# Optimization experiments

Measured on AMD Instinct MI355X. Metric: run time of the kernel, lower is better.

Reference implementation:

```python
import jax, jax.numpy as jnp
import numpy as np

SQRT_2_OVER_PI = 0.7978845608028654

def gelu_tanh(x):
    return 0.5 * x * (1.0 + jnp.tanh(SQRT_2_OVER_PI * (x + 0.044715 * x ** 3)))

def setup_inputs() -> dict:
    key = jax.random.key(0)
    ks = jax.random.split(key, 16)
    B, L, H, Dk, Dv = 4, 512, 8, 64, 64
    dm = H * Dk
    inp = {
        'q': jax.random.normal(ks[0], (B, L, dm), jnp.float32),
        'k': jax.random.normal(ks[1], (B, L, dm), jnp.float32),
        'v': jax.random.normal(ks[2], (B, L, dm), jnp.float32),
        'vec_adj_k': jax.random.normal(ks[3], (B, L, L, Dk), jnp.float32),
        'vec_adj_v': jax.random.normal(ks[4], (B, L, L, Dv), jnp.float32),
        'adj_k': jax.random.randint(ks[5], (B, L, L), 0, 2, jnp.int32),
        'adj_v': jax.random.randint(ks[6], (B, L, L), 0, 2, jnp.int32),
        # learned params (Linear weights stored as [in, out]; y = x @ W)
        'w_qs': jax.random.normal(ks[7], (dm, H * Dk), jnp.float32) * 0.02,
        'w_ks': jax.random.normal(ks[8], (dm, H * Dk), jnp.float32) * 0.02,
        'w_vs': jax.random.normal(ks[9], (dm, H * Dv), jnp.float32) * 0.02,
        'w_fc': jax.random.normal(ks[10], (H * Dk, H * Dk), jnp.float32) * 0.02,
        'w_nw': jax.random.normal(ks[11], (H * Dk, 1), jnp.float32) * 0.02,
        'w_self': jax.random.normal(ks[12], (H * Dk, H * Dk), jnp.float32) * 0.02,
        'w_dd': jax.random.normal(ks[13], (H * Dk, H * Dk), jnp.float32) * 0.02,
    }
    return inp

def reference(q, k, v, vec_adj_k, vec_adj_v, adj_k, adj_v,
              w_qs, w_ks, w_vs, w_fc, w_nw, w_self, w_dd):
    H, Dk, Dv = 8, 64, 64
    B, L, dm = q.shape
    temperature = Dk ** 0.5
    residual = q
    # projections -> [B, H, L, D]
    qh = (q @ w_qs).reshape(B, L, H, Dk).transpose(0, 2, 1, 3)
    kh = (k @ w_ks).reshape(B, L, H, Dk).transpose(0, 2, 1, 3)
    vh = (v @ w_vs).reshape(B, L, H, Dv).transpose(0, 2, 1, 3)
    qs = qh / temperature
    # inner_(q, k, vec_adj_k, flag=True): content + relative-position scores
    scores = jnp.einsum('bhld,bhmd->bhlm', qs, kh) \
           + jnp.einsum('bhld,blmd->bhlm', qs, vec_adj_k)  # [B,H,L,L]
    # adjacency mask (mask == 0 -> -10000)
    scores = jnp.where(adj_k[:, None, :, :] == 0, jnp.float32(-10000.0), scores)
    attn = jax.nn.softmax(scores, axis=-1)
    # inner_(attn, v, vec_adj_v, flag=False)
    out = jnp.einsum('bhlm,bhmd->bhld', attn, vh) \
        + jnp.einsum('bhlm,blmd->bhld', attn, vec_adj_v)
    qc = out.transpose(0, 2, 1, 3).reshape(B, L, H * Dv)  # [B,L,dm]
    # masked neighbor aggregation (GNN stage)
    adj_f = adj_k.astype(qc.dtype)
    nn_num = adj_f.sum(-1)                                  # [B,L]
    denom = jnp.where(nn_num >= 1.0, nn_num, 1.0)
    node_weight = jax.nn.sigmoid((qc @ w_nw)[..., 0])       # [B,L]
    self_info = qc @ w_self
    dd_info = qc @ w_dd
    dd_weight = node_weight[:, None, :] * adj_f             # [B,L,L]
    agg = jnp.matmul(dd_weight, dd_info) / denom[..., None]
    qo = gelu_tanh((self_info + agg) @ w_fc)
    qo = residual + qo
    return (qo, attn)
```

## Files before the change

### kernel.cpp

```cpp
#include <hip/hip_runtime.h>
#include <cstdint>

#define NB 4
#define NL 512
#define NH 8
#define ND 64
#define NDM 512

typedef __attribute__((ext_vector_type(8))) short short8;
typedef __attribute__((ext_vector_type(4))) float f32x4;

__device__ __forceinline__ unsigned short f2bf(float f){
  union { float f; unsigned u; } v; v.f = f;
  unsigned r = (v.u + 0x7fffu + ((v.u >> 16) & 1u)) >> 16;
  return (unsigned short)r;
}

__device__ __forceinline__ short8 ld8(const unsigned short* p){
  return *(const short8*)p;
}

__device__ __forceinline__ f32x4 mfma16(short8 a, short8 b, f32x4 c){
  return __builtin_amdgcn_mfma_f32_16x16x32_bf16(a, b, c, 0, 0, 0);
}

__device__ __forceinline__ float gelu_tanh(float x){
  float u = 0.7978845608028654f * (x + 0.044715f * x * x * x);
  return 0.5f * x * (1.f + tanhf(u));
}

__global__ __launch_bounds__(256) void k_cvt_in(const float* __restrict__ q,
    const float* __restrict__ k, const float* __restrict__ v,
    unsigned short* __restrict__ dst){
  int i = blockIdx.x * 256 + threadIdx.x;
  int w = i >> 18, r = i & 262143;
  const float* src = (w == 0) ? q : (w == 1) ? k : v;
  float4 f = *(const float4*)(src + (size_t)r * 4);
  unsigned lo = (unsigned)f2bf(f.x) | ((unsigned)f2bf(f.y) << 16);
  unsigned hi = (unsigned)f2bf(f.z) | ((unsigned)f2bf(f.w) << 16);
  uint2 o; o.x = lo; o.y = hi;
  *(uint2*)(dst + (size_t)w * 1048576 + (size_t)r * 4) = o;
}

__global__ __launch_bounds__(256) void k_cvt_w(const float* __restrict__ wqs,
    const float* __restrict__ wks, const float* __restrict__ wvs,
    const float* __restrict__ wself, const float* __restrict__ wdd,
    const float* __restrict__ wfc, unsigned short* __restrict__ Wt){
  int i = blockIdx.x * 256 + threadIdx.x;
  int w = i >> 18, r = i & 262143;
  const float* src = (w == 0) ? wqs : (w == 1) ? wks : (w == 2) ? wvs :
                     (w == 3) ? wself : (w == 4) ? wdd : wfc;
  int kk = r >> 9, n = r & 511;
  Wt[(size_t)w * 262144 + (size_t)n * 512 + kk] = f2bf(src[r]);
}

__global__ __launch_bounds__(256) void k_proj(const unsigned short* __restrict__ X,
    const unsigned short* __restrict__ W, unsigned short* __restrict__ dst, int mode){
  int wid = blockIdx.x * 4 + (threadIdx.x >> 6);
  int lane = threadIdx.x & 63;
  int tm = wid >> 5, tn = wid & 31;
  int r = lane & 15, q = lane >> 4;
  const unsigned short* A  = X + (size_t)(tm * 16 + r) * 512 + q * 8;
  const unsigned short* Bp = W + (size_t)(tn * 16 + r) * 512 + q * 8;
  f32x4 acc = {0.f, 0.f, 0.f, 0.f};
  for (int k = 0; k < 512; k += 32) acc = mfma16(ld8(A + k), ld8(Bp + k), acc);
  int col = tn * 16 + r;
  int h = col >> 6, d = col & 63;
  float sc = (mode == 0) ? 0.125f : 1.0f;
  for (int i = 0; i < 4; i++){
    int row = tm * 16 + q * 4 + i;
    int b = row >> 9, l = row & 511;
    float vv = acc[i] * sc;
    size_t idx = (mode == 2) ? ((size_t)((b * 8 + h) * 64 + d) * 512 + l)
                             : ((size_t)((b * 8 + h) * 512 + l) * 64 + d);
    dst[idx] = f2bf(vv);
  }
}

__global__ __launch_bounds__(256) void k_scores(const unsigned short* __restrict__ qs,
    const unsigned short* __restrict__ kh, float* __restrict__ attnF){
  int wid = blockIdx.x * 4 + (threadIdx.x >> 6);
  int lane = threadIdx.x & 63;
  int bh = wid >> 10, tile = wid & 1023;
  int tm = tile >> 5, tn = tile & 31;
  int r = lane & 15, q = lane >> 4;
  const unsigned short* A  = qs + (size_t)bh * 512 * 64 + (size_t)(tm * 16 + r) * 64 + q * 8;
  const unsigned short* Bp = kh + (size_t)bh * 512 * 64 + (size_t)(tn * 16 + r) * 64 + q * 8;
  f32x4 acc = {0.f, 0.f, 0.f, 0.f};
  acc = mfma16(ld8(A),      ld8(Bp),      acc);
  acc = mfma16(ld8(A + 32), ld8(Bp + 32), acc);
  float* C = attnF + (size_t)bh * 512 * 512;
  for (int i = 0; i < 4; i++){
    int row = tm * 16 + q * 4 + i;
    C[(size_t)row * 512 + tn * 16 + r] = acc[i];
  }
}

__global__ __launch_bounds__(256) void k_relsoft(const unsigned short* __restrict__ qs,
    const float* __restrict__ vak, const int* __restrict__ adj,
    float* __restrict__ attnF, unsigned short* __restrict__ attn_bf){
  int bid = blockIdx.x;
  int b = bid >> 9, l = bid & 511;
  int t = threadIdx.x, lane = t & 63, w = t >> 6;
  __shared__ __align__(16) unsigned short qsA[16 * 64];
  __shared__ __align__(16) unsigned short vkt[128 * 72];
  __shared__ float sc[8 * 512];
  __shared__ int adjs[512];
  for (int j = 0; j < 4; j++){
    int e = t + j * 256;
    int m = e >> 6, d = e & 63;
    qsA[e] = (m < 8) ? qs[((size_t)((b * 8 + m) * 512 + l)) * 64 + d] : (unsigned short)0;
  }
  for (int j = 0; j < 16; j++){
    int e = t + j * 256;
    int h = e >> 9, m = e & 511;
    sc[e] = attnF[((size_t)(b * 8 + h) * 512 + l) * 512 + m];
  }
  adjs[t]       = adj[(size_t)bid * 512 + t];
  adjs[t + 256] = adj[(size_t)bid * 512 + t + 256];
  __syncthreads();
  int r = lane & 15, q = lane >> 4;
  short8 a0 = ld8(qsA + r * 64 + q * 8);
  short8 a1 = ld8(qsA + r * 64 + 32 + q * 8);
  const float* vrow = vak + (size_t)bid * 512 * 64;
  for (int c = 0; c < 4; c++){
    for (int it = 0; it < 16; it++){
      int i2 = it * 256 + t;
      int m = i2 >> 5, d2 = (i2 & 31) * 2;
      const float2 f = *(const float2*)(vrow + (size_t)(c * 128 + m) * 64 + d2);
      unsigned pack = (unsigned)f2bf(f.x) | ((unsigned)f2bf(f.y) << 16);
      *(unsigned*)(&vkt[m * 72 + d2]) = pack;
    }
    __syncthreads();
    for (int nt2 = 0; nt2 < 2; nt2++){
      int nt = w * 2 + nt2;
      const unsigned short* bp = vkt + (nt * 16 + r) * 72 + q * 8;
      f32x4 acc = {0.f, 0.f, 0.f, 0.f};
      acc = mfma16(a0, ld8(bp),      acc);
      acc = mfma16(a1, ld8(bp + 32), acc);
      if (q < 2){
        for (int i = 0; i < 4; i++){
          int h = q * 4 + i;
          sc[h * 512 + c * 128 + nt * 16 + r] += acc[i];
        }
      }
    }
    __syncthreads();
  }
  for (int hh = 0; hh < 2; hh++){
    int h = w * 2 + hh;
    float v[8]; float mx = -3.0e38f;
    for (int i = 0; i < 8; i++){
      int m = lane + i * 64;
      float s = sc[h * 512 + m];
      if (adjs[m] == 0) s = -10000.0f;
      v[i] = s; mx = fmaxf(mx, s);
    }
    for (int off = 32; off; off >>= 1) mx = fmaxf(mx, __shfl_xor(mx, off, 64));
    float sum = 0.f;
    for (int i = 0; i < 8; i++){ v[i] = __expf(v[i] - mx); sum += v[i]; }
    for (int off = 32; off; off >>= 1) sum += __shfl_xor(sum, off, 64);
    float inv = 1.f / sum;
    size_t base = ((size_t)(b * 8 + h) * 512 + l) * 512;
    for (int i = 0; i < 8; i++){
      int m = lane + i * 64;
      float p2 = v[i] * inv;
      attnF[base + m] = p2;
      attn_bf[base + m] = f2bf(p2);
    }
  }
}

__global__ __launch_bounds__(256) void k_outc(const unsigned short* __restrict__ attn_bf,
    const unsigned short* __restrict__ vhT, float* __restrict__ qc){
  int wid = blockIdx.x * 4 + (threadIdx.x >> 6);
  int lane = threadIdx.x & 63;
  int bh = wid >> 7, tile = wid & 127;
  int tm = tile >> 2, tn = tile & 3;
  int r = lane & 15, q = lane >> 4;
  const unsigned short* A  = attn_bf + (size_t)bh * 512 * 512 + (size_t)(tm * 16 + r) * 512 + q * 8;
  const unsigned short* Bp = vhT + (size_t)bh * 64 * 512 + (size_t)(tn * 16 + r) * 512 + q * 8;
  f32x4 acc = {0.f, 0.f, 0.f, 0.f};
  for (int k = 0; k < 512; k += 32) acc = mfma16(ld8(A + k), ld8(Bp + k), acc);
  int b = bh >> 3, h = bh & 7;
  int d = tn * 16 + r;
  for (int i = 0; i < 4; i++){
    int lrow = tm * 16 + q * 4 + i;
    qc[(size_t)(b * 512 + lrow) * 512 + h * 64 + d] = acc[i];
  }
}

__global__ __launch_bounds__(256) void k_outrel(const unsigned short* __restrict__ attn_bf,
    const float* __restrict__ vav, const float* __restrict__ qc,
    const int* __restrict__ adj, const float* __restrict__ wnw,
    unsigned short* __restrict__ qc_bf, float* __restrict__ nw, float* __restrict__ invden){
  int bid = blockIdx.x;
  int b = bid >> 9, l = bid & 511;
  int t = threadIdx.x, lane = t & 63, w = t >> 6;
  __shared__ __align__(16) unsigned short vvT[64 * 136];
  __shared__ float orL[512];
  __shared__ float redf[4];
  __shared__ int redi[4];
  int r = lane & 15, q = lane >> 4;
  int h8 = r & 7;
  const float* vrow = vav + (size_t)bid * 512 * 64;
  const unsigned short* arow = attn_bf + ((size_t)(b * 8 + h8) * 512 + l) * 512;
  f32x4 acc = {0.f, 0.f, 0.f, 0.f};
  for (int c = 0; c < 4; c++){
    for (int it = 0; it < 16; it++){
      int i2 = it * 256 + t;
      int m = i2 >> 5, d2 = (i2 & 31) * 2;
      const float2 f = *(const float2*)(vrow + (size_t)(c * 128 + m) * 64 + d2);
      vvT[d2 * 136 + m]       = f2bf(f.x);
      vvT[(d2 + 1) * 136 + m] = f2bf(f.y);
    }
    __syncthreads();
    for (int s = 0; s < 4; s++){
      int kk = c * 128 + s * 32;
      short8 av = ld8(arow + kk + q * 8);
      short8 bv = ld8(vvT + (w * 16 + r) * 136 + s * 32 + q * 8);
      acc = mfma16(av, bv, acc);
    }
    __syncthreads();
  }
  if (q < 2){
    for (int i = 0; i < 4; i++){
      int h = q * 4 + i;
      orL[h * 64 + w * 16 + r] = acc[i];
    }
  }
  __syncthreads();
  float part = 0.f; int asum = 0;
  for (int j = 0; j < 2; j++){
    int e = t + j * 256;
    float val = qc[(size_t)bid * 512 + e] + orL[e];
    qc_bf[(size_t)bid * 512 + e] = f2bf(val);
    part += val * wnw[e];
    asum += adj[(size_t)bid * 512 + e];
  }
  for (int off = 32; off; off >>= 1){
    part += __shfl_xor(part, off, 64);
    asum += __shfl_xor(asum, off, 64);
  }
  if (lane == 0){ redf[w] = part; redi[w] = asum; }
  __syncthreads();
  if (t == 0){
    float tot = redf[0] + redf[1] + redf[2] + redf[3];
    int at = redi[0] + redi[1] + redi[2] + redi[3];
    nw[bid] = 1.f / (1.f + __expf(-tot));
    invden[bid] = 1.f / ((at >= 1) ? (float)at : 1.f);
  }
}

__global__ __launch_bounds__(256) void k_ddw(const int* __restrict__ adj,
    const float* __restrict__ nw, const float* __restrict__ invden,
    unsigned short* __restrict__ ddw){
  int i = blockIdx.x * 256 + threadIdx.x;
  int b = i >> 18, rest = i & 262143;
  int l = rest >> 9, m = rest & 511;
  int a = adj[i];
  float v = a ? nw[b * 512 + m] * invden[b * 512 + l] : 0.f;
  ddw[i] = f2bf(v);
}

__global__ __launch_bounds__(256) void k_gnn(const unsigned short* __restrict__ qcb,
    const unsigned short* __restrict__ W, float* __restrict__ outf,
    unsigned short* __restrict__ outT, int mode){
  int wid = blockIdx.x * 4 + (threadIdx.x >> 6);
  int lane = threadIdx.x & 63;
  int tm = wid >> 5, tn = wid & 31;
  int r = lane & 15, q = lane >> 4;
  const unsigned short* A  = qcb + (size_t)(tm * 16 + r) * 512 + q * 8;
  const unsigned short* Bp = W + (size_t)(tn * 16 + r) * 512 + q * 8;
  f32x4 acc = {0.f, 0.f, 0.f, 0.f};
  for (int k = 0; k < 512; k += 32) acc = mfma16(ld8(A + k), ld8(Bp + k), acc);
  int col = tn * 16 + r;
  for (int i = 0; i < 4; i++){
    int row = tm * 16 + q * 4 + i;
    if (mode == 0) outf[(size_t)row * 512 + col] = acc[i];
    else {
      int b = row >> 9, m = row & 511;
      outT[((size_t)(b * 512 + col)) * 512 + m] = f2bf(acc[i]);
    }
  }
}

__global__ __launch_bounds__(256) void k_agg(const unsigned short* __restrict__ ddw,
    const unsigned short* __restrict__ ddT, const float* __restrict__ selfi,
    unsigned short* __restrict__ xbf){
  int wid = blockIdx.x * 4 + (threadIdx.x >> 6);
  int lane = threadIdx.x & 63;
  int b = wid >> 10, tile = wid & 1023;
  int tm = tile >> 5, tn = tile & 31;
  int r = lane & 15, q = lane >> 4;
  const unsigned short* A  = ddw + (size_t)b * 262144 + (size_t)(tm * 16 + r) * 512 + q * 8;
  const unsigned short* Bp = ddT + (size_t)b * 262144 + (size_t)(tn * 16 + r) * 512 + q * 8;
  f32x4 acc = {0.f, 0.f, 0.f, 0.f};
  for (int k = 0; k < 512; k += 32) acc = mfma16(ld8(A + k), ld8(Bp + k), acc);
  int col = tn * 16 + r;
  for (int i = 0; i < 4; i++){
    int row = b * 512 + tm * 16 + q * 4 + i;
    float x = acc[i] + selfi[(size_t)row * 512 + col];
    xbf[(size_t)row * 512 + col] = f2bf(x);
  }
}

__global__ __launch_bounds__(256) void k_fc(const unsigned short* __restrict__ xbf,
    const unsigned short* __restrict__ W, const float* __restrict__ qin,
    float* __restrict__ qo){
  int wid = blockIdx.x * 4 + (threadIdx.x >> 6);
  int lane = threadIdx.x & 63;
  int tm = wid >> 5, tn = wid & 31;
  int r = lane & 15, q = lane >> 4;
  const unsigned short* A  = xbf + (size_t)(tm * 16 + r) * 512 + q * 8;
  const unsigned short* Bp = W + (size_t)(tn * 16 + r) * 512 + q * 8;
  f32x4 acc = {0.f, 0.f, 0.f, 0.f};
  for (int k = 0; k < 512; k += 32) acc = mfma16(ld8(A + k), ld8(Bp + k), acc);
  int col = tn * 16 + r;
  for (int i = 0; i < 4; i++){
    int row = tm * 16 + q * 4 + i;
    qo[(size_t)row * 512 + col] = qin[(size_t)row * 512 + col] + gelu_tanh(acc[i]);
  }
}

extern "C" void kernel_launch(void* const* d_in, const int* in_sizes, int n_in,
                              void* d_out, int out_size, void* d_ws, size_t ws_size,
                              hipStream_t stream){
  const float* q    = (const float*)d_in[0];
  const float* k    = (const float*)d_in[1];
  const float* v    = (const float*)d_in[2];
  const float* vak  = (const float*)d_in[3];
  const float* vav  = (const float*)d_in[4];
  const int*   adjk = (const int*)d_in[5];
  const float* wqs  = (const float*)d_in[7];
  const float* wks  = (const float*)d_in[8];
  const float* wvs  = (const float*)d_in[9];
  const float* wfc  = (const float*)d_in[10];
  const float* wnw  = (const float*)d_in[11];
  const float* wself= (const float*)d_in[12];
  const float* wdd  = (const float*)d_in[13];

  float* qo    = (float*)d_out;
  float* attnF = qo + 1048576;

  char* p = (char*)d_ws;
  unsigned short* xin   = (unsigned short*)p; p += 6291456;
  unsigned short* Wt    = (unsigned short*)p; p += 3145728;
  unsigned short* qsb   = (unsigned short*)p; p += 2097152;
  unsigned short* khb   = (unsigned short*)p; p += 2097152;
  unsigned short* vhT   = (unsigned short*)p; p += 2097152;
  unsigned short* attnb = (unsigned short*)p; p += 16777216;
  float*          qc    = (float*)p;          p += 4194304;
  unsigned short* qcb   = (unsigned short*)p; p += 2097152;
  float*          nw    = (float*)p;          p += 8192;
  float*          invd  = (float*)p;          p += 8192;
  float*          selfi = (float*)p;          p += 4194304;
  unsigned short* ddT   = (unsigned short*)p; p += 2097152;
  unsigned short* ddw   = (unsigned short*)p; p += 2097152;
  unsigned short* xbf   = (unsigned short*)p; p += 2097152;

  k_cvt_in<<<3072, 256, 0, stream>>>(q, k, v, xin);
  k_cvt_w<<<6144, 256, 0, stream>>>(wqs, wks, wvs, wself, wdd, wfc, Wt);
  k_proj<<<1024, 256, 0, stream>>>(xin,           Wt,          qsb, 0);
  k_proj<<<1024, 256, 0, stream>>>(xin + 1048576, Wt + 262144, khb, 1);
  k_proj<<<1024, 256, 0, stream>>>(xin + 2097152, Wt + 524288, vhT, 2);
  k_scores<<<8192, 256, 0, stream>>>(qsb, khb, attnF);
  k_relsoft<<<2048, 256, 0, stream>>>(qsb, vak, adjk, attnF, attnb);
  k_outc<<<1024, 256, 0, stream>>>(attnb, vhT, qc);
  k_outrel<<<2048, 256, 0, stream>>>(attnb, vav, qc, adjk, wnw, qcb, nw, invd);
  k_ddw<<<4096, 256, 0, stream>>>(adjk, nw, invd, ddw);
  k_gnn<<<1024, 256, 0, stream>>>(qcb, Wt + 786432,  selfi, (unsigned short*)nullptr, 0);
  k_gnn<<<1024, 256, 0, stream>>>(qcb, Wt + 1048576, (float*)nullptr, ddT, 1);
  k_agg<<<1024, 256, 0, stream>>>(ddw, ddT, selfi, xbf);
  k_fc<<<1024, 256, 0, stream>>>(xbf, Wt + 1310720, q, qo);
}
```

Baseline: 736.5 us.

## Merge small kernels, vectorize loads, and reuse Q fragments in score kernel

Merges the input and weight conversion kernels into one launch, the three projections into one launch, and the self/dd GEMMs plus ddw construction into one launch. This cuts launch count and tail effects. The weight transpose now writes packed 16-byte rows, and the dd output transpose is staged through LDS so global stores are coalesced. The score kernel reuses the loaded Q fragments across four N tiles. The relsoft and outrel kernels load vec_adj with float4 instead of float2.

```diff
diff --git a/kernel.cpp b/kernel.cpp
--- a/kernel.cpp
+++ b/kernel.cpp
@@ -29,41 +29,64 @@
   return 0.5f * x * (1.f + tanhf(u));
 }
 
-__global__ __launch_bounds__(256) void k_cvt_in(const float* __restrict__ q,
+__global__ __launch_bounds__(256) void k_prep(const float* __restrict__ q,
     const float* __restrict__ k, const float* __restrict__ v,
-    unsigned short* __restrict__ dst){
-  int i = blockIdx.x * 256 + threadIdx.x;
-  int w = i >> 18, r = i & 262143;
-  const float* src = (w == 0) ? q : (w == 1) ? k : v;
-  float4 f = *(const float4*)(src + (size_t)r * 4);
-  unsigned lo = (unsigned)f2bf(f.x) | ((unsigned)f2bf(f.y) << 16);
-  unsigned hi = (unsigned)f2bf(f.z) | ((unsigned)f2bf(f.w) << 16);
-  uint2 o; o.x = lo; o.y = hi;
-  *(uint2*)(dst + (size_t)w * 1048576 + (size_t)r * 4) = o;
-}
-
-__global__ __launch_bounds__(256) void k_cvt_w(const float* __restrict__ wqs,
-    const float* __restrict__ wks, const float* __restrict__ wvs,
-    const float* __restrict__ wself, const float* __restrict__ wdd,
-    const float* __restrict__ wfc, unsigned short* __restrict__ Wt){
-  int i = blockIdx.x * 256 + threadIdx.x;
-  int w = i >> 18, r = i & 262143;
-  const float* src = (w == 0) ? wqs : (w == 1) ? wks : (w == 2) ? wvs :
-                     (w == 3) ? wself : (w == 4) ? wdd : wfc;
-  int kk = r >> 9, n = r & 511;
-  Wt[(size_t)w * 262144 + (size_t)n * 512 + kk] = f2bf(src[r]);
-}
-
-__global__ __launch_bounds__(256) void k_proj(const unsigned short* __restrict__ X,
-    const unsigned short* __restrict__ W, unsigned short* __restrict__ dst, int mode){
-  int wid = blockIdx.x * 4 + (threadIdx.x >> 6);
+    unsigned short* __restrict__ xin,
+    const float* __restrict__ wqs, const float* __restrict__ wks,
+    const float* __restrict__ wvs, const float* __restrict__ wself,
+    const float* __restrict__ wdd, const float* __restrict__ wfc,
+    unsigned short* __restrict__ Wt){
+  int blk = blockIdx.x;
+  int t = threadIdx.x;
+  if (blk < 3072){
+    int i = blk * 256 + t;
+    int w = i >> 18, r = i & 262143;
+    const float* src = (w == 0) ? q : (w == 1) ? k : v;
+    float4 f = *(const float4*)(src + (size_t)r * 4);
+    unsigned lo = (unsigned)f2bf(f.x) | ((unsigned)f2bf(f.y) << 16);
+    unsigned hi = (unsigned)f2bf(f.z) | ((unsigned)f2bf(f.w) << 16);
+    uint2 o; o.x = lo; o.y = hi;
+    *(uint2*)(xin + (size_t)w * 1048576 + (size_t)r * 4) = o;
+  } else {
+    int i = (blk - 3072) * 256 + t;
+    int w = i >> 13;
+    int rr = i & 8191;
+    int kg = rr >> 9;
+    int n  = rr & 511;
+    int k0 = kg * 32;
+    const float* src = (w == 0) ? wqs : (w == 1) ? wks : (w == 2) ? wvs :
+                       (w == 3) ? wself : (w == 4) ? wdd : wfc;
+    unsigned pk[16];
+#pragma unroll
+    for (int j = 0; j < 16; j++){
+      float a = src[(size_t)(k0 + 2 * j) * 512 + n];
+      float b = src[(size_t)(k0 + 2 * j + 1) * 512 + n];
+      pk[j] = (unsigned)f2bf(a) | ((unsigned)f2bf(b) << 16);
+    }
+    uint4* o4 = (uint4*)(Wt + (size_t)w * 262144 + (size_t)n * 512 + k0);
+    o4[0] = make_uint4(pk[0],  pk[1],  pk[2],  pk[3]);
+    o4[1] = make_uint4(pk[4],  pk[5],  pk[6],  pk[7]);
+    o4[2] = make_uint4(pk[8],  pk[9],  pk[10], pk[11]);
+    o4[3] = make_uint4(pk[12], pk[13], pk[14], pk[15]);
+  }
+}
+
+__global__ __launch_bounds__(256) void k_proj(const unsigned short* __restrict__ xin,
+    const unsigned short* __restrict__ Wt, unsigned short* __restrict__ qsb,
+    unsigned short* __restrict__ khb, unsigned short* __restrict__ vhT){
+  int wid0 = blockIdx.x * 4 + (threadIdx.x >> 6);
+  int mode = wid0 >> 10;
+  int wid = wid0 & 1023;
   int lane = threadIdx.x & 63;
   int tm = wid >> 5, tn = wid & 31;
   int r = lane & 15, q = lane >> 4;
+  const unsigned short* X = xin + (size_t)mode * 1048576;
+  const unsigned short* W = Wt + (size_t)mode * 262144;
+  unsigned short* dst = (mode == 0) ? qsb : (mode == 1) ? khb : vhT;
   const unsigned short* A  = X + (size_t)(tm * 16 + r) * 512 + q * 8;
   const unsigned short* Bp = W + (size_t)(tn * 16 + r) * 512 + q * 8;
   f32x4 acc = {0.f, 0.f, 0.f, 0.f};
-  for (int k = 0; k < 512; k += 32) acc = mfma16(ld8(A + k), ld8(Bp + k), acc);
+  for (int kk = 0; kk < 512; kk += 32) acc = mfma16(ld8(A + kk), ld8(Bp + kk), acc);
   int col = tn * 16 + r;
   int h = col >> 6, d = col & 63;
   float sc = (mode == 0) ? 0.125f : 1.0f;
@@ -81,18 +104,22 @@
     const unsigned short* __restrict__ kh, float* __restrict__ attnF){
   int wid = blockIdx.x * 4 + (threadIdx.x >> 6);
   int lane = threadIdx.x & 63;
-  int bh = wid >> 10, tile = wid & 1023;
-  int tm = tile >> 5, tn = tile & 31;
-  int r = lane & 15, q = lane >> 4;
-  const unsigned short* A  = qs + (size_t)bh * 512 * 64 + (size_t)(tm * 16 + r) * 64 + q * 8;
-  const unsigned short* Bp = kh + (size_t)bh * 512 * 64 + (size_t)(tn * 16 + r) * 64 + q * 8;
-  f32x4 acc = {0.f, 0.f, 0.f, 0.f};
-  acc = mfma16(ld8(A),      ld8(Bp),      acc);
-  acc = mfma16(ld8(A + 32), ld8(Bp + 32), acc);
+  int bh = wid >> 8;
+  int rest = wid & 255;
+  int tm = rest >> 3, tg = rest & 7;
+  int r = lane & 15, q = lane >> 4;
+  const unsigned short* A = qs + (size_t)bh * 512 * 64 + (size_t)(tm * 16 + r) * 64 + q * 8;
+  short8 a0 = ld8(A), a1 = ld8(A + 32);
   float* C = attnF + (size_t)bh * 512 * 512;
-  for (int i = 0; i < 4; i++){
-    int row = tm * 16 + q * 4 + i;
-    C[(size_t)row * 512 + tn * 16 + r] = acc[i];
+  for (int tn = tg * 4; tn < tg * 4 + 4; tn++){
+    const unsigned short* Bp = kh + (size_t)bh * 512 * 64 + (size_t)(tn * 16 + r) * 64 + q * 8;
+    f32x4 acc = {0.f, 0.f, 0.f, 0.f};
+    acc = mfma16(a0, ld8(Bp),      acc);
+    acc = mfma16(a1, ld8(Bp + 32), acc);
+    for (int i = 0; i < 4; i++){
+      int row = tm * 16 + q * 4 + i;
+      C[(size_t)row * 512 + tn * 16 + r] = acc[i];
+    }
   }
 }
 
@@ -124,12 +151,14 @@
   short8 a1 = ld8(qsA + r * 64 + 32 + q * 8);
   const float* vrow = vak + (size_t)bid * 512 * 64;
   for (int c = 0; c < 4; c++){
-    for (int it = 0; it < 16; it++){
-      int i2 = it * 256 + t;
-      int m = i2 >> 5, d2 = (i2 & 31) * 2;
-      const float2 f = *(const float2*)(vrow + (size_t)(c * 128 + m) * 64 + d2);
-      unsigned pack = (unsigned)f2bf(f.x) | ((unsigned)f2bf(f.y) << 16);
-      *(unsigned*)(&vkt[m * 72 + d2]) = pack;
+    for (int it = 0; it < 8; it++){
+      int i4 = it * 256 + t;
+      int m = i4 >> 4, d4 = (i4 & 15) * 4;
+      const float4 f = *(const float4*)(vrow + (size_t)(c * 128 + m) * 64 + d4);
+      unsigned p0 = (unsigned)f2bf(f.x) | ((unsigned)f2bf(f.y) << 16);
+      unsigned p1 = (unsigned)f2bf(f.z) | ((unsigned)f2bf(f.w) << 16);
+      uint2 pp; pp.x = p0; pp.y = p1;
+      *(uint2*)(&vkt[m * 72 + d4]) = pp;
     }
     __syncthreads();
     for (int nt2 = 0; nt2 < 2; nt2++){
@@ -207,12 +236,14 @@
   const unsigned short* arow = attn_bf + ((size_t)(b * 8 + h8) * 512 + l) * 512;
   f32x4 acc = {0.f, 0.f, 0.f, 0.f};
   for (int c = 0; c < 4; c++){
-    for (int it = 0; it < 16; it++){
-      int i2 = it * 256 + t;
-      int m = i2 >> 5, d2 = (i2 & 31) * 2;
-      const float2 f = *(const float2*)(vrow + (size_t)(c * 128 + m) * 64 + d2);
-      vvT[d2 * 136 + m]       = f2bf(f.x);
-      vvT[(d2 + 1) * 136 + m] = f2bf(f.y);
+    for (int it = 0; it < 8; it++){
+      int i4 = it * 256 + t;
+      int m = i4 >> 4, d4 = (i4 & 15) * 4;
+      const float4 f = *(const float4*)(vrow + (size_t)(c * 128 + m) * 64 + d4);
+      vvT[(d4    ) * 136 + m] = f2bf(f.x);
+      vvT[(d4 + 1) * 136 + m] = f2bf(f.y);
+      vvT[(d4 + 2) * 136 + m] = f2bf(f.z);
+      vvT[(d4 + 3) * 136 + m] = f2bf(f.w);
     }
     __syncthreads();
     for (int s = 0; s < 4; s++){
@@ -252,36 +283,52 @@
   }
 }
 
-__global__ __launch_bounds__(256) void k_ddw(const int* __restrict__ adj,
-    const float* __restrict__ nw, const float* __restrict__ invden,
-    unsigned short* __restrict__ ddw){
-  int i = blockIdx.x * 256 + threadIdx.x;
-  int b = i >> 18, rest = i & 262143;
-  int l = rest >> 9, m = rest & 511;
-  int a = adj[i];
-  float v = a ? nw[b * 512 + m] * invden[b * 512 + l] : 0.f;
-  ddw[i] = f2bf(v);
-}
-
-__global__ __launch_bounds__(256) void k_gnn(const unsigned short* __restrict__ qcb,
-    const unsigned short* __restrict__ W, float* __restrict__ outf,
-    unsigned short* __restrict__ outT, int mode){
-  int wid = blockIdx.x * 4 + (threadIdx.x >> 6);
-  int lane = threadIdx.x & 63;
-  int tm = wid >> 5, tn = wid & 31;
-  int r = lane & 15, q = lane >> 4;
-  const unsigned short* A  = qcb + (size_t)(tm * 16 + r) * 512 + q * 8;
-  const unsigned short* Bp = W + (size_t)(tn * 16 + r) * 512 + q * 8;
-  f32x4 acc = {0.f, 0.f, 0.f, 0.f};
-  for (int k = 0; k < 512; k += 32) acc = mfma16(ld8(A + k), ld8(Bp + k), acc);
-  int col = tn * 16 + r;
-  for (int i = 0; i < 4; i++){
-    int row = tm * 16 + q * 4 + i;
-    if (mode == 0) outf[(size_t)row * 512 + col] = acc[i];
-    else {
-      int b = row >> 9, m = row & 511;
-      outT[((size_t)(b * 512 + col)) * 512 + m] = f2bf(acc[i]);
-    }
+__global__ __launch_bounds__(256) void k_post(const unsigned short* __restrict__ qcb,
+    const unsigned short* __restrict__ Wself, const unsigned short* __restrict__ Wdd,
+    float* __restrict__ selfi, unsigned short* __restrict__ ddT,
+    const int* __restrict__ adj, const float* __restrict__ nw,
+    const float* __restrict__ invden, unsigned short* __restrict__ ddw){
+  __shared__ __align__(16) unsigned short ldsT[64 * 20];
+  int blk = blockIdx.x;
+  int t = threadIdx.x;
+  if (blk < 2048){
+    int mode = blk >> 10;
+    int wv = t >> 6;
+    int wid = (blk & 1023) * 4 + wv;
+    int lane = t & 63;
+    int tm = wid >> 5, tn = wid & 31;
+    int r = lane & 15, q = lane >> 4;
+    const unsigned short* W = mode ? Wdd : Wself;
+    const unsigned short* A  = qcb + (size_t)(tm * 16 + r) * 512 + q * 8;
+    const unsigned short* Bp = W + (size_t)(tn * 16 + r) * 512 + q * 8;
+    f32x4 acc = {0.f, 0.f, 0.f, 0.f};
+    for (int kk = 0; kk < 512; kk += 32) acc = mfma16(ld8(A + kk), ld8(Bp + kk), acc);
+    int col = tn * 16 + r;
+    if (mode == 0){
+      for (int i = 0; i < 4; i++){
+        int row = tm * 16 + q * 4 + i;
+        selfi[(size_t)row * 512 + col] = acc[i];
+      }
+    } else {
+      int nLocal = wv * 16 + r;
+      for (int i = 0; i < 4; i++) ldsT[nLocal * 20 + q * 4 + i] = f2bf(acc[i]);
+      __syncthreads();
+      int tmB = ((blk & 1023) * 4) >> 5;
+      int tnBase = ((blk & 1023) * 4) & 31;
+      int n = t >> 2, part = t & 3;
+      ushort4 val = *(const ushort4*)(&ldsT[n * 20 + part * 4]);
+      int b = (tmB * 16) >> 9;
+      int m0 = (tmB * 16) & 511;
+      int nGlob = tnBase * 16 + n;
+      *(ushort4*)(&ddT[((size_t)(b * 512 + nGlob)) * 512 + m0 + part * 4]) = val;
+    }
+  } else {
+    int i = (blk - 2048) * 256 + t;
+    int b = i >> 18, rest = i & 262143;
+    int l = rest >> 9, m = rest & 511;
+    int a = adj[i];
+    float v = a ? nw[b * 512 + m] * invden[b * 512 + l] : 0.f;
+    ddw[i] = f2bf(v);
   }
 }
 
@@ -359,18 +406,14 @@
   unsigned short* ddw   = (unsigned short*)p; p += 2097152;
   unsigned short* xbf   = (unsigned short*)p; p += 2097152;
 
-  k_cvt_in<<<3072, 256, 0, stream>>>(q, k, v, xin);
-  k_cvt_w<<<6144, 256, 0, stream>>>(wqs, wks, wvs, wself, wdd, wfc, Wt);
-  k_proj<<<1024, 256, 0, stream>>>(xin,           Wt,          qsb, 0);
-  k_proj<<<1024, 256, 0, stream>>>(xin + 1048576, Wt + 262144, khb, 1);
-  k_proj<<<1024, 256, 0, stream>>>(xin + 2097152, Wt + 524288, vhT, 2);
-  k_scores<<<8192, 256, 0, stream>>>(qsb, khb, attnF);
+  k_prep<<<3264, 256, 0, stream>>>(q, k, v, xin, wqs, wks, wvs, wself, wdd, wfc, Wt);
+  k_proj<<<3072, 256, 0, stream>>>(xin, Wt, qsb, khb, vhT);
+  k_scores<<<2048, 256, 0, stream>>>(qsb, khb, attnF);
   k_relsoft<<<2048, 256, 0, stream>>>(qsb, vak, adjk, attnF, attnb);
   k_outc<<<1024, 256, 0, stream>>>(attnb, vhT, qc);
   k_outrel<<<2048, 256, 0, stream>>>(attnb, vav, qc, adjk, wnw, qcb, nw, invd);
-  k_ddw<<<4096, 256, 0, stream>>>(adjk, nw, invd, ddw);
-  k_gnn<<<1024, 256, 0, stream>>>(qcb, Wt + 786432,  selfi, (unsigned short*)nullptr, 0);
-  k_gnn<<<1024, 256, 0, stream>>>(qcb, Wt + 1048576, (float*)nullptr, ddT, 1);
+  k_post<<<6144, 256, 0, stream>>>(qcb, Wt + 786432, Wt + 1048576, selfi, ddT,
+                                   adjk, nw, invd, ddw);
   k_agg<<<1024, 256, 0, stream>>>(ddw, ddT, selfi, xbf);
   k_fc<<<1024, 256, 0, stream>>>(xbf, Wt + 1310720, q, qo);
 }
```

Measured after the change: 713.7 us. -3.1%, faster.
